# Optimization experiments

Measured on AMD Instinct MI355X. Metric: run time of the kernel, lower is better.

Reference implementation:

```python
import jax, jax.numpy as jnp
import numpy as np

KERNEL_MUL = 2.0
KERNEL_NUM = 5

N_S = 4096
N_T = 4096
D = 512
N_CLS = 10


def setup_inputs() -> dict:
    key = jax.random.key(0)
    k1, k2, k3 = jax.random.split(key, 3)
    x = jax.random.normal(k1, (N_S + N_T, D), dtype=jnp.float32)
    # source-first domain labels: first N_S are source (0), rest target (1)
    domain_labels = jnp.concatenate(
        [jnp.zeros((N_S,), dtype=jnp.int32), jnp.ones((N_T,), dtype=jnp.int32)]
    )
    y_true = jax.random.randint(k2, (N_S,), 0, N_CLS, dtype=jnp.int32)
    im_weights = jax.random.uniform(k3, (N_CLS,), dtype=jnp.float32, minval=0.5, maxval=1.5)
    return {
        "x": x,
        "im_weights": im_weights,
        "domain_labels": domain_labels,
        "y_true": y_true,
        "alpha": 1,
    }


def _gaussian_kernel_sum(total, n_samples):
    # Pairwise squared L2 distances via Gram trick instead of the O(N^2*D)
    # broadcasted tensor the torch code materializes (same math).
    sq = jnp.sum(total * total, axis=1)                      # [N]
    l2 = sq[:, None] + sq[None, :] - 2.0 * (total @ total.T)  # [N, N]
    l2 = jnp.maximum(l2, 0.0)
    # bandwidth computed on detached distances (torch uses L2_distance.data)
    bandwidth = jnp.sum(jax.lax.stop_gradient(l2)) / float(n_samples * n_samples - n_samples)
    bandwidth = bandwidth / (KERNEL_MUL ** (KERNEL_NUM // 2))
    k = jnp.zeros_like(l2)
    for i in range(KERNEL_NUM):
        k = k + jnp.exp(-l2 / (bandwidth * (KERNEL_MUL ** i)))
    return k


def reference(x, im_weights, domain_labels, y_true, alpha):
    dl = np.asarray(domain_labels)  # int labels are concrete constants
    src = np.where(dl == 0)[0]
    tgt = np.where(dl == 1)[0]
    n_s, n_t = len(src), len(tgt)

    total = jnp.concatenate([x[src], x[tgt]], axis=0)        # [n_s+n_t, D]
    kernels = _gaussian_kernel_sum(total, n_s + n_t)         # [N, N]

    # importance weights are detached in the torch code
    iw = jax.lax.stop_gradient(alpha * im_weights + (1.0 - alpha))
    w = iw[y_true]                                           # [n_s]

    k_ss = kernels[:n_s, :n_s]
    k_tt = kernels[n_s:, n_s:]
    k_st = kernels[:n_s, n_s:]

    # loss_1: weighted source upper-triangle + unweighted target upper-triangle
    loss_1 = jnp.sum(jnp.triu(k_ss * (w[:, None] * w[None, :]), k=1)) / float(n_s * (n_s - 1) / 2)
    loss_1 = loss_1 + jnp.sum(jnp.triu(k_tt, k=1)) / float(n_t * (n_t - 1) / 2)

    # loss_2: cross term, weighted by source sample weights
    loss_2 = jnp.sum(k_st * w[:, None]) / float(n_s * n_t)

    return loss_1 - 2.0 * loss_2
```

## Files before the change

kernel.cpp:

```cpp
#include <hip/hip_runtime.h>
#include <math.h>

#define N_TOT 8192
#define N_SRC 4096
#define D_DIM 512
#define BM 128
#define NT (N_TOT / BM)
#define NTILES (NT * (NT + 1) / 2)
#define NPREP 256

typedef short bf16x8 __attribute__((ext_vector_type(8)));
typedef unsigned short u16x8 __attribute__((ext_vector_type(8)));
typedef float f32x4 __attribute__((ext_vector_type(4)));


__device__ __forceinline__ unsigned short f2bf_rn(float v) {
    unsigned int u = __float_as_uint(v);
    unsigned int r = (u + 0x7FFFu + ((u >> 16) & 1u)) >> 16;
    return (unsigned short)r;
}

__global__ __launch_bounds__(256) void k_prep(const float* __restrict__ x,
                                              unsigned short* __restrict__ xhi,
                                              float* __restrict__ sq,
                                              float* __restrict__ colpart) {
    const int wave = threadIdx.x >> 6;
    const int lane = threadIdx.x & 63;
    __shared__ float colbuf[4][512];
    float fcol[8];
#pragma unroll
    for (int j = 0; j < 8; ++j) fcol[j] = 0.f;

#pragma unroll
    for (int r8 = 0; r8 < 8; ++r8) {
        const int row = blockIdx.x * 32 + wave * 8 + r8;
        const size_t base = (size_t)row * D_DIM + lane * 8;
        float v[8];
        *(float4*)&v[0] = *(const float4*)(x + base);
        *(float4*)&v[4] = *(const float4*)(x + base + 4);
        u16x8 h;
        float s = 0.f;
#pragma unroll
        for (int j = 0; j < 8; ++j) {
            h[j] = f2bf_rn(v[j]);
            s = fmaf(v[j], v[j], s);
            fcol[j] += v[j];
        }
        *(u16x8*)(xhi + base) = h;
#pragma unroll
        for (int off = 32; off; off >>= 1) s += __shfl_xor(s, off);
        if (lane == 0) sq[row] = s;
    }
#pragma unroll
    for (int j = 0; j < 8; ++j) colbuf[wave][lane * 8 + j] = fcol[j];
    __syncthreads();
    const int c = threadIdx.x * 2;
    float2 r;
    r.x = colbuf[0][c] + colbuf[1][c] + colbuf[2][c] + colbuf[3][c];
    r.y = colbuf[0][c + 1] + colbuf[1][c + 1] + colbuf[2][c + 1] + colbuf[3][c + 1];
    *(float2*)(colpart + (size_t)blockIdx.x * D_DIM + c) = r;
}

__global__ __launch_bounds__(256) void k_bw(const float* __restrict__ sq,
                                            const float* __restrict__ colpart,
                                            const float* __restrict__ imw,
                                            const int* __restrict__ y,
                                            const int* __restrict__ alpha_p,
                                            float* __restrict__ w,
                                            float* __restrict__ invbw,
                                            double* __restrict__ accum,
                                            unsigned int* __restrict__ cnt) {
    const int tid = threadIdx.x;
    if (tid == 0) { accum[2] = 0.0; *cnt = 0u; }
    const float a = (float)alpha_p[0];
    for (int i = tid; i < N_SRC; i += 256) w[i] = a * imw[y[i]] + (1.0f - a);
    double s2 = 0.0;
    for (int i = tid; i < N_TOT; i += 256) s2 += (double)sq[i];
    double cs0 = 0.0, cs1 = 0.0;
    const int c = tid * 2;
#pragma unroll 8
    for (int b = 0; b < NPREP; ++b) {
        float2 v = *(const float2*)(colpart + (size_t)b * D_DIM + c);
        cs0 += (double)v.x;
        cs1 += (double)v.y;
    }
    double sc = cs0 * cs0 + cs1 * cs1;
    __shared__ double r1[256], r2[256];
    r1[tid] = s2; r2[tid] = sc;
    __syncthreads();
    for (int off = 128; off; off >>= 1) {
        if (tid < off) { r1[tid] += r1[tid + off]; r2[tid] += r2[tid + off]; }
        __syncthreads();
    }
    if (tid == 0) {
        double sum_l2 = 2.0 * (double)N_TOT * r1[0] - 2.0 * r2[0];
        double bw = sum_l2 / ((double)N_TOT * (double)N_TOT - (double)N_TOT);
        bw *= 0.25;
        double m = 1.0;
        for (int i = 0; i < 5; ++i) { invbw[i] = (float)(1.0 / (bw * m)); m *= 2.0; }
    }
}

__device__ __forceinline__ void gload_lds16(const unsigned short* g, char* l) {
    __builtin_amdgcn_global_load_lds((const __attribute__((address_space(1))) void*)g,
                                     (__attribute__((address_space(3))) void*)l,
                                     16, 0, 0);
}

__device__ __forceinline__ int swz_of(int row) { return (row & 3) ^ ((row >> 2) & 3); }

__global__ __launch_bounds__(256, 3) void k_pairs(const unsigned short* __restrict__ xhi,
                                                  const float* __restrict__ sq,
                                                  const float* __restrict__ w,
                                                  const float* __restrict__ invbw,
                                                  double* __restrict__ accum,
                                                  unsigned int* __restrict__ cnt,
                                                  float* __restrict__ out) {
    int bid = (blockIdx.x & 7) * (NTILES / 8) + (blockIdx.x >> 3);
    int ti = 0, rem = bid;
    while (rem >= NT - ti) { rem -= NT - ti; ++ti; }
    const int tj = ti + rem;
    const int i0 = ti * BM, j0 = tj * BM;

    __shared__ __align__(16) char lds[3 * 16384];
    __shared__ double sdl4[4];

    const int tid = threadIdx.x;
    const int lane = tid & 63;
    const int wave = tid >> 6;
    const int wr = wave >> 1, wc = wave & 1;
    const int lr = lane & 15, lg = lane >> 4;

    f32x4 acc[4][4];
#pragma unroll
    for (int m = 0; m < 4; ++m)
#pragma unroll
        for (int n = 0; n < 4; ++n) acc[m][n] = f32x4{0.f, 0.f, 0.f, 0.f};

    const unsigned short* srcs[2] = {xhi + (size_t)i0 * D_DIM, xhi + (size_t)j0 * D_DIM};

#define STAGE(P, KK)                                                                   \
    do {                                                                               \
        _Pragma("unroll") for (int t4 = 0; t4 < 4; ++t4) {                             \
            int idx = t4 * 256 + tid;                                                  \
            int tile = idx >> 9;                                                       \
            int ci = idx & 511;                                                        \
            int row = ci >> 2, cc = ci & 3;                                            \
            int cg = cc ^ swz_of(row);                                                 \
            gload_lds16(srcs[tile] + (size_t)row * D_DIM + (KK) + cg * 8,              \
                        lds + (P) * 16384 + idx * 16);                                 \
        }                                                                              \
    } while (0)

    STAGE(0, 0);
    STAGE(1, 32);
    asm volatile("s_waitcnt vmcnt(4)\n\ts_barrier" ::: "memory");
    __builtin_amdgcn_sched_barrier(0);

#pragma unroll
    for (int t = 0; t < 16; ++t) {
        const int cur = t % 3;
        if (t < 14) STAGE((t + 2) % 3, (t + 2) * 32);

        const char* lAh = lds + cur * 16384;
        const char* lBh = lAh + 8192;
        bf16x8 ah[4], bh[4];
#pragma unroll
        for (int m = 0; m < 4; ++m) {
            int row = wr * 64 + m * 16 + lr;
            int off = row * 64 + ((lg ^ swz_of(row)) << 4);
            ah[m] = *(const bf16x8*)(lAh + off);
        }
#pragma unroll
        for (int n = 0; n < 4; ++n) {
            int row = wc * 64 + n * 16 + lr;
            int off = row * 64 + ((lg ^ swz_of(row)) << 4);
            bh[n] = *(const bf16x8*)(lBh + off);
        }
        __builtin_amdgcn_s_setprio(1);
#pragma unroll
        for (int m = 0; m < 4; ++m)
#pragma unroll
            for (int n = 0; n < 4; ++n)
                acc[m][n] = __builtin_amdgcn_mfma_f32_16x16x32_bf16(ah[m], bh[n], acc[m][n], 0, 0, 0);
        __builtin_amdgcn_s_setprio(0);

        if (t < 14) {
            asm volatile("s_waitcnt lgkmcnt(0) vmcnt(4)\n\ts_barrier" ::: "memory");
            __builtin_amdgcn_sched_barrier(0);
        } else if (t == 14) {
            asm volatile("s_waitcnt lgkmcnt(0) vmcnt(0)\n\ts_barrier" ::: "memory");
            __builtin_amdgcn_sched_barrier(0);
        }
    }
#undef STAGE

    float sqi[4][4], wi[4][4], sqj[4], wj[4];
#pragma unroll
    for (int m = 0; m < 4; ++m)
#pragma unroll
        for (int j = 0; j < 4; ++j) {
            int i = i0 + wr * 64 + m * 16 + lg * 4 + j;
            sqi[m][j] = sq[i];
            wi[m][j] = (i < N_SRC) ? w[i] : 0.f;
        }
#pragma unroll
    for (int n = 0; n < 4; ++n) {
        int jg = j0 + wc * 64 + n * 16 + lr;
        sqj[n] = sq[jg];
        wj[n] = (jg < N_SRC) ? w[jg] : 0.f;
    }
    const float nib4 = -invbw[4];

    const bool diag = (ti == tj);
    const int region = (tj < NT / 2) ? 0 : ((ti >= NT / 2) ? 1 : 2);

    float facc = 0.f;
#pragma unroll
    for (int m = 0; m < 4; ++m)
#pragma unroll
        for (int n = 0; n < 4; ++n)
#pragma unroll
            for (int j = 0; j < 4; ++j) {
                int rg = wr * 64 + m * 16 + lg * 4 + j;
                int cg = wc * 64 + n * 16 + lr;
                if (diag && rg >= cg) continue;
                float l2 = fmaf(-2.f, acc[m][n][j], sqi[m][j] + sqj[n]);
                l2 = fmaxf(l2, 0.f);
                float t = __expf(l2 * nib4);
                float t2 = t * t, t4 = t2 * t2, t8 = t4 * t4, t16 = t8 * t8;
                float k5 = t + t2 + t4 + t8 + t16;
                float cf;
                if (region == 0)      cf = wi[m][j] * wj[n];
                else if (region == 1) cf = 1.f;
                else                  cf = wi[m][j];
                facc = fmaf(k5, cf, facc);
            }

#pragma unroll
    for (int off = 32; off; off >>= 1) facc += __shfl_xor(facc, off);
    if (lane == 0) sdl4[wave] = (double)facc;
    __syncthreads();
    if (tid == 0) {
        const double C_SS = 1.0 / 8386560.0;
        const double C_ST = 2.0 / 16777216.0;
        double scale = (region == 2) ? -C_ST : C_SS;
        atomicAdd(&accum[2], scale * (sdl4[0] + sdl4[1] + sdl4[2] + sdl4[3]));
        __threadfence();
        unsigned int old = atomicAdd(cnt, 1u);
        if (old == NTILES - 1) {
            double v = atomicAdd(&accum[2], 0.0);
            out[0] = (float)v;
        }
    }
}

extern "C" void kernel_launch(void* const* d_in, const int* in_sizes, int n_in,
                              void* d_out, int out_size, void* d_ws, size_t ws_size,
                              hipStream_t stream) {
    const float* x    = (const float*)d_in[0];
    const float* imw  = (const float*)d_in[1];
    const int*   y    = (const int*)d_in[3];
    const int*   alph = (const int*)d_in[4];
    float* out = (float*)d_out;

    char* ws = (char*)d_ws;
    double*       accum   = (double*)ws;
    unsigned int* cnt     = (unsigned int*)(ws + 64);
    float*        invbw   = (float*)(ws + 128);
    float*        sq      = (float*)(ws + 4096);
    float*        wgt     = (float*)(ws + 36864);
    float*        colpart = (float*)(ws + 53248);
    unsigned short* xhi   = (unsigned short*)(ws + 577536);

    k_prep<<<NPREP, 256, 0, stream>>>(x, xhi, sq, colpart);
    k_bw<<<1, 256, 0, stream>>>(sq, colpart, imw, y, alph, wgt, invbw, accum, cnt);
    k_pairs<<<NTILES, 256, 0, stream>>>(xhi, sq, wgt, invbw, accum, cnt, out);
}
```

Baseline: 188.2 us.

## Load MFMA operands directly from global memory instead of LDS staging

```diff
diff --git a/kernel.cpp b/kernel.cpp
--- a/kernel.cpp
+++ b/kernel.cpp
@@ -101,28 +101,19 @@
     }
 }
 
-__device__ __forceinline__ void gload_lds16(const unsigned short* g, char* l) {
-    __builtin_amdgcn_global_load_lds((const __attribute__((address_space(1))) void*)g,
-                                     (__attribute__((address_space(3))) void*)l,
-                                     16, 0, 0);
-}
-
-__device__ __forceinline__ int swz_of(int row) { return (row & 3) ^ ((row >> 2) & 3); }
-
-__global__ __launch_bounds__(256, 3) void k_pairs(const unsigned short* __restrict__ xhi,
-                                                  const float* __restrict__ sq,
-                                                  const float* __restrict__ w,
-                                                  const float* __restrict__ invbw,
-                                                  double* __restrict__ accum,
-                                                  unsigned int* __restrict__ cnt,
-                                                  float* __restrict__ out) {
+__global__ __launch_bounds__(256) void k_pairs(const unsigned short* __restrict__ xhi,
+                                               const float* __restrict__ sq,
+                                               const float* __restrict__ w,
+                                               const float* __restrict__ invbw,
+                                               double* __restrict__ accum,
+                                               unsigned int* __restrict__ cnt,
+                                               float* __restrict__ out) {
     int bid = (blockIdx.x & 7) * (NTILES / 8) + (blockIdx.x >> 3);
     int ti = 0, rem = bid;
     while (rem >= NT - ti) { rem -= NT - ti; ++ti; }
     const int tj = ti + rem;
     const int i0 = ti * BM, j0 = tj * BM;
 
-    __shared__ __align__(16) char lds[3 * 16384];
     __shared__ double sdl4[4];
 
     const int tid = threadIdx.x;
@@ -137,63 +128,42 @@
 #pragma unroll
         for (int n = 0; n < 4; ++n) acc[m][n] = f32x4{0.f, 0.f, 0.f, 0.f};
 
-    const unsigned short* srcs[2] = {xhi + (size_t)i0 * D_DIM, xhi + (size_t)j0 * D_DIM};
-
-#define STAGE(P, KK)                                                                   \
-    do {                                                                               \
-        _Pragma("unroll") for (int t4 = 0; t4 < 4; ++t4) {                             \
-            int idx = t4 * 256 + tid;                                                  \
-            int tile = idx >> 9;                                                       \
-            int ci = idx & 511;                                                        \
-            int row = ci >> 2, cc = ci & 3;                                            \
-            int cg = cc ^ swz_of(row);                                                 \
-            gload_lds16(srcs[tile] + (size_t)row * D_DIM + (KK) + cg * 8,              \
-                        lds + (P) * 16384 + idx * 16);                                 \
-        }                                                                              \
-    } while (0)
-
-    STAGE(0, 0);
-    STAGE(1, 32);
-    asm volatile("s_waitcnt vmcnt(4)\n\ts_barrier" ::: "memory");
-    __builtin_amdgcn_sched_barrier(0);
-
-#pragma unroll
-    for (int t = 0; t < 16; ++t) {
-        const int cur = t % 3;
-        if (t < 14) STAGE((t + 2) % 3, (t + 2) * 32);
-
-        const char* lAh = lds + cur * 16384;
-        const char* lBh = lAh + 8192;
-        bf16x8 ah[4], bh[4];
+    const unsigned short* aRow = xhi + (size_t)(i0 + wr * 64 + lr) * D_DIM + lg * 8;
+    const unsigned short* bRow = xhi + (size_t)(j0 + wc * 64 + lr) * D_DIM + lg * 8;
+
+    bf16x8 aA[4], bA[4], aB[4], bB[4];
+#pragma unroll
+    for (int m = 0; m < 4; ++m) {
+        aA[m] = *(const bf16x8*)(aRow + m * 16 * D_DIM);
+        bA[m] = *(const bf16x8*)(bRow + m * 16 * D_DIM);
+    }
+#pragma unroll
+    for (int t = 0; t < 16; t += 2) {
+        const int k1 = (t + 1) * 32;
 #pragma unroll
         for (int m = 0; m < 4; ++m) {
-            int row = wr * 64 + m * 16 + lr;
-            int off = row * 64 + ((lg ^ swz_of(row)) << 4);
-            ah[m] = *(const bf16x8*)(lAh + off);
-        }
-#pragma unroll
-        for (int n = 0; n < 4; ++n) {
-            int row = wc * 64 + n * 16 + lr;
-            int off = row * 64 + ((lg ^ swz_of(row)) << 4);
-            bh[n] = *(const bf16x8*)(lBh + off);
-        }
-        __builtin_amdgcn_s_setprio(1);
+            aB[m] = *(const bf16x8*)(aRow + m * 16 * D_DIM + k1);
+            bB[m] = *(const bf16x8*)(bRow + m * 16 * D_DIM + k1);
+        }
 #pragma unroll
         for (int m = 0; m < 4; ++m)
 #pragma unroll
             for (int n = 0; n < 4; ++n)
-                acc[m][n] = __builtin_amdgcn_mfma_f32_16x16x32_bf16(ah[m], bh[n], acc[m][n], 0, 0, 0);
-        __builtin_amdgcn_s_setprio(0);
-
-        if (t < 14) {
-            asm volatile("s_waitcnt lgkmcnt(0) vmcnt(4)\n\ts_barrier" ::: "memory");
-            __builtin_amdgcn_sched_barrier(0);
-        } else if (t == 14) {
-            asm volatile("s_waitcnt lgkmcnt(0) vmcnt(0)\n\ts_barrier" ::: "memory");
-            __builtin_amdgcn_sched_barrier(0);
-        }
-    }
-#undef STAGE
+                acc[m][n] = __builtin_amdgcn_mfma_f32_16x16x32_bf16(aA[m], bA[n], acc[m][n], 0, 0, 0);
+        if (t + 2 < 16) {
+            const int k2 = (t + 2) * 32;
+#pragma unroll
+            for (int m = 0; m < 4; ++m) {
+                aA[m] = *(const bf16x8*)(aRow + m * 16 * D_DIM + k2);
+                bA[m] = *(const bf16x8*)(bRow + m * 16 * D_DIM + k2);
+            }
+        }
+#pragma unroll
+        for (int m = 0; m < 4; ++m)
+#pragma unroll
+            for (int n = 0; n < 4; ++n)
+                acc[m][n] = __builtin_amdgcn_mfma_f32_16x16x32_bf16(aB[m], bB[n], acc[m][n], 0, 0, 0);
+    }
 
     float sqi[4][4], wi[4][4], sqj[4], wj[4];
 #pragma unroll
```

New measurement: 291.1 us. 1.55x slower.
